# Performance work log

Measured on AMD Instinct MI355X. Metric: run time of the kernel, lower is better.

The kernel has to match this reference:

```python
import jax, jax.numpy as jnp
import numpy as np

EMBED_DIM = 768
NUM_HEADS = 12
HEAD_DIM = EMBED_DIM // NUM_HEADS


def setup_inputs() -> dict:
    key = jax.random.key(0)
    ks = jax.random.split(key, 9)
    B, S, E = 8, 1024, EMBED_DIM
    scale = 1.0 / np.sqrt(E)
    inputs = jax.random.normal(ks[0], (B, S, E), dtype=jnp.float32)
    Wq = jax.random.normal(ks[1], (E, E), dtype=jnp.float32) * scale
    Wk = jax.random.normal(ks[2], (E, E), dtype=jnp.float32) * scale
    Wv = jax.random.normal(ks[3], (E, E), dtype=jnp.float32) * scale
    Wo = jax.random.normal(ks[4], (E, E), dtype=jnp.float32) * scale
    bq = jnp.zeros((E,), dtype=jnp.float32)
    bk = jnp.zeros((E,), dtype=jnp.float32)
    bv = jnp.zeros((E,), dtype=jnp.float32)
    bo = jnp.zeros((E,), dtype=jnp.float32)
    return {"inputs": inputs, "Wq": Wq, "bq": bq, "Wk": Wk, "bk": bk,
            "Wv": Wv, "bv": bv, "Wo": Wo, "bo": bo}


def reference(inputs, Wq, bq, Wk, bk, Wv, bv, Wo, bo):
    B, S, E = inputs.shape
    H, D = NUM_HEADS, HEAD_DIM

    def split_heads(x):  # [B,S,E] -> [B,H,S,D]
        return x.reshape(B, S, H, D).transpose(0, 2, 1, 3)

    q = split_heads(inputs @ Wq + bq)
    k = split_heads(inputs @ Wk + bk)
    v = split_heads(inputs @ Wv + bv)

    # scaled dot-product attention; note: scale uses sqrt(last dim of key) = sqrt(D)
    score = jnp.einsum('bhqd,bhkd->bhqk', q, k) / jnp.sqrt(jnp.float32(D))
    weights = jax.nn.softmax(score, axis=-1)
    attn = jnp.einsum('bhqk,bhkd->bhqd', weights, v)  # [B,H,S,D]

    concat = attn.transpose(0, 2, 1, 3).reshape(B, S, E)
    return concat @ Wo + bo
```

## Files before the change

### kernel.cpp

```cpp
#include <hip/hip_runtime.h>
#include <hip/hip_bf16.h>
#include <cstddef>

#define E_DIM  768
#define S_LEN  1024
#define NHEADS 12
#define HDIM   64
#define BATCH  8
#define TOKENS (BATCH * S_LEN)
#define WELEMS (E_DIM * E_DIM)

typedef short bf16x8 __attribute__((ext_vector_type(8)));
typedef short bf16x4 __attribute__((ext_vector_type(4)));
typedef float f32x4  __attribute__((ext_vector_type(4)));

#define MFMA16(a, b, c)   __builtin_amdgcn_mfma_f32_16x16x32_bf16((a), (b), (c), 0, 0, 0)
#define MFMA16K16(a, b, c) __builtin_amdgcn_mfma_f32_16x16x16bf16_1k((a), (b), (c), 0, 0, 0)

#define GLD_LDS16(gp, lp)                                                  \
    __builtin_amdgcn_global_load_lds(                                      \
        (const __attribute__((address_space(1))) void*)(gp),               \
        (__attribute__((address_space(3))) void*)(lp), 16, 0, 0)

#define QSCALE 0.180336880f

static __device__ __forceinline__ short f2bf(float f) {
    union { float f; unsigned int u; } cv; cv.f = f;
    unsigned int u = cv.u + 0x7fffu + ((cv.u >> 16) & 1u);
    return (short)(u >> 16);
}

static __device__ __forceinline__ unsigned int pk2(float f0, float f1) {
    union { float f; unsigned int u; } a, b;
    a.f = f0; b.f = f1;
    return __builtin_amdgcn_perm(b.u + 0x8000u, a.u + 0x8000u, 0x07060302u);
}
static __device__ __forceinline__ bf16x4 pk4(float f0, float f1, float f2, float f3) {
    union { unsigned int u[2]; bf16x4 v; } r;
    r.u[0] = pk2(f0, f1); r.u[1] = pk2(f2, f3);
    return r.v;
}

__global__ __launch_bounds__(256) void xcvt_kernel(
    const float* __restrict__ X, short* __restrict__ Y)
{
    const size_t i = ((size_t)blockIdx.x * 256 + threadIdx.x) * 8;
    const float4 a = *(const float4*)&X[i];
    const float4 b = *(const float4*)&X[i + 4];
    union { unsigned int u[4]; bf16x8 v; } o;
    o.u[0] = pk2(a.x, a.y); o.u[1] = pk2(a.z, a.w);
    o.u[2] = pk2(b.x, b.y); o.u[3] = pk2(b.z, b.w);
    *(bf16x8*)&Y[i] = o.v;
}

__global__ __launch_bounds__(256) void transpose_w(
    const float* __restrict__ s0, const float* __restrict__ s1,
    const float* __restrict__ s2, const float* __restrict__ s3,
    short* __restrict__ dst)
{
    const int z = blockIdx.z;
    const float* S = (z == 0) ? s0 : (z == 1) ? s1 : (z == 2) ? s2 : s3;
    short* D = dst + (size_t)z * WELEMS;
    __shared__ float t[64][65];
    const int r = threadIdx.x >> 2, c0 = (threadIdx.x & 3) * 16;
    const int br = blockIdx.x * 64, bc = blockIdx.y * 64;
    #pragma unroll
    for (int j = 0; j < 4; ++j) {
        float4 v = *(const float4*)&S[(size_t)(br + r) * E_DIM + bc + c0 + j * 4];
        t[r][c0 + j * 4 + 0] = v.x; t[r][c0 + j * 4 + 1] = v.y;
        t[r][c0 + j * 4 + 2] = v.z; t[r][c0 + j * 4 + 3] = v.w;
    }
    __syncthreads();
    #pragma unroll
    for (int half = 0; half < 2; ++half) {
        union { unsigned int u[2]; bf16x4 v; } o0, o1;
        o0.u[0] = pk2(t[c0 + half * 8 + 0][r], t[c0 + half * 8 + 1][r]);
        o0.u[1] = pk2(t[c0 + half * 8 + 2][r], t[c0 + half * 8 + 3][r]);
        o1.u[0] = pk2(t[c0 + half * 8 + 4][r], t[c0 + half * 8 + 5][r]);
        o1.u[1] = pk2(t[c0 + half * 8 + 6][r], t[c0 + half * 8 + 7][r]);
        *(bf16x4*)&D[(size_t)(bc + r) * E_DIM + br + c0 + half * 8]     = o0.v;
        *(bf16x4*)&D[(size_t)(bc + r) * E_DIM + br + c0 + half * 8 + 4] = o1.v;
    }
}

template<bool AF32>
__global__ __launch_bounds__(256, 3) void gemm_qkv_t(
    const void* __restrict__ Ap, const short* __restrict__ Wt,
    const float* __restrict__ bq, const float* __restrict__ bk,
    const float* __restrict__ bv, short* __restrict__ oq,
    short* __restrict__ ok, short* __restrict__ ov)
{
    __shared__ __align__(16) short As[128 * 64];
    __shared__ __align__(16) short Bs[128 * 64];

    const int tid  = threadIdx.x;
    const int wave = tid >> 6, lane = tid & 63;
    const int quad = lane >> 4, l16 = lane & 15;
    const int bid = blockIdx.x;
    const int xcd = bid & 7, qq = bid >> 3;
    const int nblk = qq >> 3;
    const int bm = (xcd * 8 + (qq & 7)) * 128;
    const int wsel = nblk / 6;
    const int nb = (nblk % 6) * 128;
    const short* wt = Wt + (size_t)wsel * WELEMS;
    const float* bias = (wsel == 0) ? bq : (wsel == 1) ? bk : bv;
    short* outp = (wsel == 0) ? oq : (wsel == 1) ? ok : ov;
    const int wm = (wave >> 1) * 64, wn = (wave & 1) * 64;

    f32x4 acc[4][4];
    #pragma unroll
    for (int mt = 0; mt < 4; ++mt)
        #pragma unroll
        for (int nt = 0; nt < 4; ++nt) acc[mt][nt] = (f32x4){0.f, 0.f, 0.f, 0.f};

    for (int k0 = 0; k0 < E_DIM; k0 += 64) {
        if (AF32) {
            const float* A = (const float*)Ap;
            float4 ax[4][2];
            #pragma unroll
            for (int i = 0; i < 4; ++i) {
                const int slot = i * 256 + tid;
                const int row = slot >> 3, cl = slot & 7;
                const float4* gp = (const float4*)&A[(size_t)(bm + row) * E_DIM + k0 + cl * 8];
                ax[i][0] = gp[0]; ax[i][1] = gp[1];
            }
            __syncthreads();
            #pragma unroll
            for (int i = 0; i < 4; ++i) {
                const int slot = i * 256 + tid;
                const int row = slot >> 3, cl = slot & 7, cg = cl ^ (row & 7);
                GLD_LDS16(&wt[(size_t)(nb + row) * E_DIM + k0 + cg * 8], &Bs[slot * 8]);
            }
            #pragma unroll
            for (int i = 0; i < 4; ++i) {
                const int slot = i * 256 + tid;
                const int row = slot >> 3, cl = slot & 7, cs = cl ^ (row & 7);
                union { unsigned int u[4]; bf16x8 v; } v8;
                v8.u[0] = pk2(ax[i][0].x, ax[i][0].y);
                v8.u[1] = pk2(ax[i][0].z, ax[i][0].w);
                v8.u[2] = pk2(ax[i][1].x, ax[i][1].y);
                v8.u[3] = pk2(ax[i][1].z, ax[i][1].w);
                *(bf16x8*)&As[row * 64 + cs * 8] = v8.v;
            }
        } else {
            const short* A = (const short*)Ap;
            __syncthreads();
            #pragma unroll
            for (int i = 0; i < 4; ++i) {
                const int slot = i * 256 + tid;
                const int row = slot >> 3, cl = slot & 7, cg = cl ^ (row & 7);
                GLD_LDS16(&A[(size_t)(bm + row) * E_DIM + k0 + cg * 8], &As[slot * 8]);
            }
            #pragma unroll
            for (int i = 0; i < 4; ++i) {
                const int slot = i * 256 + tid;
                const int row = slot >> 3, cl = slot & 7, cg = cl ^ (row & 7);
                GLD_LDS16(&wt[(size_t)(nb + row) * E_DIM + k0 + cg * 8], &Bs[slot * 8]);
            }
        }
        __syncthreads();

        #pragma unroll
        for (int ks = 0; ks < 2; ++ks) {
            bf16x8 a[4], b[4];
            #pragma unroll
            for (int mt = 0; mt < 4; ++mt) {
                const int row = wm + mt * 16 + l16;
                const int c = (ks * 4 + quad) ^ (row & 7);
                a[mt] = *(const bf16x8*)&As[row * 64 + c * 8];
            }
            #pragma unroll
            for (int nt = 0; nt < 4; ++nt) {
                const int row = wn + nt * 16 + l16;
                const int c = (ks * 4 + quad) ^ (row & 7);
                b[nt] = *(const bf16x8*)&Bs[row * 64 + c * 8];
            }
            #pragma unroll
            for (int mt = 0; mt < 4; ++mt)
                #pragma unroll
                for (int nt = 0; nt < 4; ++nt)
                    acc[mt][nt] = MFMA16(a[mt], b[nt], acc[mt][nt]);
        }
    }

    const float qscale = (wsel == 0) ? QSCALE : 1.0f;
    #pragma unroll
    for (int nt = 0; nt < 4; ++nt) {
        const int ncol = nb + wn + nt * 16 + l16;
        const float bvv = bias[ncol];
        const int h = ncol >> 6, d = ncol & (HDIM - 1);
        #pragma unroll
        for (int mt = 0; mt < 4; ++mt) {
            const int grow = bm + wm + mt * 16 + quad * 4;
            if (wsel == 1) {
                #pragma unroll
                for (int r = 0; r < 4; ++r) {
                    const int g = grow + r, b = g >> 10, s = g & (S_LEN - 1);
                    outp[((size_t)(b * NHEADS + h) * S_LEN + s) * HDIM + d] =
                        f2bf(acc[mt][nt][r] + bvv);
                }
            } else {
                const int b = grow >> 10, s0 = grow & (S_LEN - 1);
                bf16x4 pv = pk4((acc[mt][nt][0] + bvv) * qscale,
                                (acc[mt][nt][1] + bvv) * qscale,
                                (acc[mt][nt][2] + bvv) * qscale,
                                (acc[mt][nt][3] + bvv) * qscale);
                *(bf16x4*)&outp[((size_t)(b * NHEADS + h) * HDIM + d) * S_LEN + s0] = pv;
            }
        }
    }
}

__global__ __launch_bounds__(256, 3) void gemm_out_kernel(
    const short* __restrict__ A, const short* __restrict__ Wt,
    const float* __restrict__ bias, float* __restrict__ out)
{
    __shared__ __align__(16) short As[128 * 64];
    __shared__ __align__(16) short Bs[128 * 64];

    const int tid  = threadIdx.x;
    const int wave = tid >> 6, lane = tid & 63;
    const int quad = lane >> 4, l16 = lane & 15;
    const int bid = blockIdx.x;
    const int xcd = bid & 7, qq = bid >> 3;
    const int nb = (qq >> 3) * 128;
    const int bm = (xcd * 8 + (qq & 7)) * 128;
    const int wm = (wave >> 1) * 64, wn = (wave & 1) * 64;

    f32x4 acc[4][4];
    #pragma unroll
    for (int mt = 0; mt < 4; ++mt)
        #pragma unroll
        for (int nt = 0; nt < 4; ++nt) acc[mt][nt] = (f32x4){0.f, 0.f, 0.f, 0.f};

    for (int k0 = 0; k0 < E_DIM; k0 += 64) {
        __syncthreads();
        #pragma unroll
        for (int i = 0; i < 4; ++i) {
            const int slot = i * 256 + tid;
            const int row = slot >> 3, cl = slot & 7, cg = cl ^ (row & 7);
            GLD_LDS16(&A[(size_t)(bm + row) * E_DIM + k0 + cg * 8], &As[slot * 8]);
        }
        #pragma unroll
        for (int i = 0; i < 4; ++i) {
            const int slot = i * 256 + tid;
            const int row = slot >> 3, cl = slot & 7, cg = cl ^ (row & 7);
            GLD_LDS16(&Wt[(size_t)(nb + row) * E_DIM + k0 + cg * 8], &Bs[slot * 8]);
        }
        __syncthreads();

        #pragma unroll
        for (int ks = 0; ks < 2; ++ks) {
            bf16x8 a[4], b[4];
            #pragma unroll
            for (int mt = 0; mt < 4; ++mt) {
                const int row = wm + mt * 16 + l16;
                const int c = (ks * 4 + quad) ^ (row & 7);
                a[mt] = *(const bf16x8*)&As[row * 64 + c * 8];
            }
            #pragma unroll
            for (int nt = 0; nt < 4; ++nt) {
                const int row = wn + nt * 16 + l16;
                const int c = (ks * 4 + quad) ^ (row & 7);
                b[nt] = *(const bf16x8*)&Bs[row * 64 + c * 8];
            }
            #pragma unroll
            for (int mt = 0; mt < 4; ++mt)
                #pragma unroll
                for (int nt = 0; nt < 4; ++nt)
                    acc[mt][nt] = MFMA16(a[mt], b[nt], acc[mt][nt]);
        }
    }

    #pragma unroll
    for (int nt = 0; nt < 4; ++nt) {
        const int ncol = nb + wn + nt * 16 + l16;
        const float bvv = bias[ncol];
        #pragma unroll
        for (int mt = 0; mt < 4; ++mt) {
            const int grow = bm + wm + mt * 16 + quad * 4;
            #pragma unroll
            for (int r = 0; r < 4; ++r)
                out[(size_t)(grow + r) * E_DIM + ncol] = acc[mt][nt][r] + bvv;
        }
    }
}

__global__ __launch_bounds__(256) void attn_kernel(
    const short* __restrict__ Q, const short* __restrict__ K,
    const short* __restrict__ V, short* __restrict__ O)
{
    __shared__ __align__(16) short Ks[2][64 * 64];
    __shared__ __align__(16) short Vt[2][64 * 64];

    const int tid  = threadIdx.x;
    const int wave = tid >> 6, lane = tid & 63;
    const int quad = lane >> 4, l16 = lane & 15;
    const int bh = blockIdx.x;
    const int q0 = blockIdx.y * 128;
    const size_t base = (size_t)bh * S_LEN * HDIM;
    const short* Qb = Q + base;
    const short* Kb = K + base;
    const short* Vb = V + base;

    bf16x8 qa[2][2];
    #pragma unroll
    for (int mt = 0; mt < 2; ++mt)
        #pragma unroll
        for (int ks = 0; ks < 2; ++ks) {
            const int s = q0 + wave * 32 + mt * 16 + l16;
            #pragma unroll
            for (int j = 0; j < 8; ++j)
                qa[mt][ks][j] = Qb[(size_t)(ks * 32 + quad * 8 + j) * S_LEN + s];
        }

    bf16x4 ones4;
    #pragma unroll
    for (int j = 0; j < 4; ++j) ones4[j] = (short)0x3F80;

    f32x4 oacc[2][4], lacc[2];
    #pragma unroll
    for (int mt = 0; mt < 2; ++mt) {
        #pragma unroll
        for (int nt = 0; nt < 4; ++nt) oacc[mt][nt] = (f32x4){0.f, 0.f, 0.f, 0.f};
        lacc[mt] = (f32x4){0.f, 0.f, 0.f, 0.f};
    }

    #pragma unroll
    for (int i = 0; i < 2; ++i) {
        const int slot = i * 256 + tid;
        const int row = slot >> 3, cl = slot & 7, cg = cl ^ (row & 7);
        GLD_LDS16(&Kb[(size_t)row * HDIM + cg * 8], &Ks[0][slot * 8]);
        GLD_LDS16(&Vb[(size_t)row * S_LEN + cg * 8], &Vt[0][slot * 8]);
    }

    for (int it = 0; it < S_LEN / 64; ++it) {
        __syncthreads();
        if (it + 1 < S_LEN / 64) {
            const int kt = (it + 1) * 64, nbf = (it + 1) & 1;
            #pragma unroll
            for (int i = 0; i < 2; ++i) {
                const int slot = i * 256 + tid;
                const int row = slot >> 3, cl = slot & 7, cg = cl ^ (row & 7);
                GLD_LDS16(&Kb[(size_t)(kt + row) * HDIM + cg * 8], &Ks[nbf][slot * 8]);
                GLD_LDS16(&Vb[(size_t)row * S_LEN + kt + cg * 8], &Vt[nbf][slot * 8]);
            }
        }
        const short* ksb = Ks[it & 1];
        const short* vtb = Vt[it & 1];

        f32x4 sc[2][4];
        #pragma unroll
        for (int mt = 0; mt < 2; ++mt)
            #pragma unroll
            for (int t = 0; t < 4; ++t) sc[mt][t] = (f32x4){0.f, 0.f, 0.f, 0.f};
        #pragma unroll
        for (int ks = 0; ks < 2; ++ks)
            #pragma unroll
            for (int t = 0; t < 4; ++t) {
                const int row = t * 16 + l16;
                const int c = (ks * 4 + quad) ^ (row & 7);
                const bf16x8 kf = *(const bf16x8*)&ksb[row * 64 + c * 8];
                #pragma unroll
                for (int mt = 0; mt < 2; ++mt)
                    sc[mt][t] = MFMA16(kf, qa[mt][ks], sc[mt][t]);
            }

        bf16x4 pa16[2][4];
        #pragma unroll
        for (int mt = 0; mt < 2; ++mt)
            #pragma unroll
            for (int t = 0; t < 4; ++t)
                pa16[mt][t] = pk4(__builtin_amdgcn_exp2f(sc[mt][t][0]),
                                  __builtin_amdgcn_exp2f(sc[mt][t][1]),
                                  __builtin_amdgcn_exp2f(sc[mt][t][2]),
                                  __builtin_amdgcn_exp2f(sc[mt][t][3]));

        #pragma unroll
        for (int t = 0; t < 4; ++t) {
            #pragma unroll
            for (int mt = 0; mt < 2; ++mt)
                lacc[mt] = MFMA16K16(pa16[mt][t], ones4, lacc[mt]);
            #pragma unroll
            for (int nt = 0; nt < 4; ++nt) {
                const int row = nt * 16 + l16;
                const int c = (t * 2 + (quad >> 1)) ^ (row & 7);
                const bf16x4 vb = *(const bf16x4*)&vtb[row * 64 + c * 8 + (quad & 1) * 4];
                #pragma unroll
                for (int mt = 0; mt < 2; ++mt)
                    oacc[mt][nt] = MFMA16K16(pa16[mt][t], vb, oacc[mt][nt]);
            }
        }
    }

    const int b = bh / NHEADS, h = bh - b * NHEADS;
    #pragma unroll
    for (int mt = 0; mt < 2; ++mt)
        #pragma unroll
        for (int nt = 0; nt < 4; ++nt)
            #pragma unroll
            for (int r = 0; r < 4; ++r) {
                const int qrow = q0 + wave * 32 + mt * 16 + quad * 4 + r;
                const float val = oacc[mt][nt][r] / lacc[mt][r];
                O[(size_t)(b * S_LEN + qrow) * E_DIM + h * HDIM + nt * 16 + l16] = f2bf(val);
            }
}

extern "C" void kernel_launch(void* const* d_in, const int* in_sizes, int n_in,
                              void* d_out, int out_size, void* d_ws, size_t ws_size,
                              hipStream_t stream) {
    const float* X  = (const float*)d_in[0];
    const float* Wq = (const float*)d_in[1];
    const float* bq = (const float*)d_in[2];
    const float* Wk = (const float*)d_in[3];
    const float* bk = (const float*)d_in[4];
    const float* Wv = (const float*)d_in[5];
    const float* bv = (const float*)d_in[6];
    const float* Wo = (const float*)d_in[7];
    const float* bo = (const float*)d_in[8];
    float* out = (float*)d_out;

    const size_t t = (size_t)TOKENS * E_DIM;
    short* q    = (short*)d_ws;
    short* k    = q + t;
    short* vT   = k + t;
    short* attn = vT + t;

    const size_t fast_need = (5 * t + 4 * (size_t)WELEMS) * 2;
    if (ws_size >= fast_need) {
        short* wt4 = attn + t;
        short* xbf = wt4 + 4 * (size_t)WELEMS;
        xcvt_kernel<<<(TOKENS * E_DIM / 8) / 256, 256, 0, stream>>>(X, xbf);
        transpose_w<<<dim3(12, 12, 4), 256, 0, stream>>>(Wq, Wk, Wv, Wo, wt4);
        gemm_qkv_t<false><<<1152, 256, 0, stream>>>(
            xbf, wt4, bq, bk, bv, q, k, vT);
        attn_kernel<<<dim3(BATCH * NHEADS, S_LEN / 128), 256, 0, stream>>>(q, k, vT, attn);
        gemm_out_kernel<<<384, 256, 0, stream>>>(
            attn, wt4 + 3 * (size_t)WELEMS, bo, out);
    } else {
        short* wt_qkv = attn;
        short* wt_o   = q;
        transpose_w<<<dim3(12, 12, 3), 256, 0, stream>>>(Wq, Wk, Wv, Wv, wt_qkv);
        gemm_qkv_t<true><<<1152, 256, 0, stream>>>(
            X, wt_qkv, bq, bk, bv, q, k, vT);
        attn_kernel<<<dim3(BATCH * NHEADS, S_LEN / 128), 256, 0, stream>>>(q, k, vT, attn);
        transpose_w<<<dim3(12, 12, 1), 256, 0, stream>>>(Wo, Wo, Wo, Wo, wt_o);
        gemm_out_kernel<<<384, 256, 0, stream>>>(attn, wt_o, bo, out);
    }
}
```

Measured before the change: 191.6 us.

## Double-buffer LDS tiles in QKV and output projection GEMMs

Adds a second LDS buffer for the A and B tiles in both projection GEMMs. The next k-tile is issued before computing on the current one, so global loads overlap MFMA work and one barrier per iteration is dropped. This doubles shared memory per block, which can reduce how many blocks fit on a CU. In the fp32-input path the synchronous register loads still stall before compute.

```diff
diff --git a/kernel.cpp b/kernel.cpp
--- a/kernel.cpp
+++ b/kernel.cpp
@@ -90,8 +90,8 @@
     const float* __restrict__ bv, short* __restrict__ oq,
     short* __restrict__ ok, short* __restrict__ ov)
 {
-    __shared__ __align__(16) short As[128 * 64];
-    __shared__ __align__(16) short Bs[128 * 64];
+    __shared__ __align__(16) short As[2][128 * 64];
+    __shared__ __align__(16) short Bs[2][128 * 64];
 
     const int tid  = threadIdx.x;
     const int wave = tid >> 6, lane = tid & 63;
@@ -113,52 +113,53 @@
         #pragma unroll
         for (int nt = 0; nt < 4; ++nt) acc[mt][nt] = (f32x4){0.f, 0.f, 0.f, 0.f};
 
-    for (int k0 = 0; k0 < E_DIM; k0 += 64) {
+    const int NIT = E_DIM / 64;
+
+    auto stage = [&](int it, int bf) {
+        const int k0 = it * 64;
         if (AF32) {
             const float* A = (const float*)Ap;
-            float4 ax[4][2];
-            #pragma unroll
-            for (int i = 0; i < 4; ++i) {
-                const int slot = i * 256 + tid;
-                const int row = slot >> 3, cl = slot & 7;
-                const float4* gp = (const float4*)&A[(size_t)(bm + row) * E_DIM + k0 + cl * 8];
-                ax[i][0] = gp[0]; ax[i][1] = gp[1];
-            }
-            __syncthreads();
             #pragma unroll
             for (int i = 0; i < 4; ++i) {
                 const int slot = i * 256 + tid;
                 const int row = slot >> 3, cl = slot & 7, cg = cl ^ (row & 7);
-                GLD_LDS16(&wt[(size_t)(nb + row) * E_DIM + k0 + cg * 8], &Bs[slot * 8]);
+                GLD_LDS16(&wt[(size_t)(nb + row) * E_DIM + k0 + cg * 8], &Bs[bf][slot * 8]);
             }
             #pragma unroll
             for (int i = 0; i < 4; ++i) {
                 const int slot = i * 256 + tid;
                 const int row = slot >> 3, cl = slot & 7, cs = cl ^ (row & 7);
+                const float4* gp = (const float4*)&A[(size_t)(bm + row) * E_DIM + k0 + cl * 8];
+                const float4 a0 = gp[0], a1 = gp[1];
                 union { unsigned int u[4]; bf16x8 v; } v8;
-                v8.u[0] = pk2(ax[i][0].x, ax[i][0].y);
-                v8.u[1] = pk2(ax[i][0].z, ax[i][0].w);
-                v8.u[2] = pk2(ax[i][1].x, ax[i][1].y);
-                v8.u[3] = pk2(ax[i][1].z, ax[i][1].w);
-                *(bf16x8*)&As[row * 64 + cs * 8] = v8.v;
+                v8.u[0] = pk2(a0.x, a0.y); v8.u[1] = pk2(a0.z, a0.w);
+                v8.u[2] = pk2(a1.x, a1.y); v8.u[3] = pk2(a1.z, a1.w);
+                *(bf16x8*)&As[bf][row * 64 + cs * 8] = v8.v;
             }
         } else {
             const short* A = (const short*)Ap;
-            __syncthreads();
             #pragma unroll
             for (int i = 0; i < 4; ++i) {
                 const int slot = i * 256 + tid;
                 const int row = slot >> 3, cl = slot & 7, cg = cl ^ (row & 7);
-                GLD_LDS16(&A[(size_t)(bm + row) * E_DIM + k0 + cg * 8], &As[slot * 8]);
+                GLD_LDS16(&A[(size_t)(bm + row) * E_DIM + k0 + cg * 8], &As[bf][slot * 8]);
             }
             #pragma unroll
             for (int i = 0; i < 4; ++i) {
                 const int slot = i * 256 + tid;
                 const int row = slot >> 3, cl = slot & 7, cg = cl ^ (row & 7);
-                GLD_LDS16(&wt[(size_t)(nb + row) * E_DIM + k0 + cg * 8], &Bs[slot * 8]);
-            }
-        }
+                GLD_LDS16(&wt[(size_t)(nb + row) * E_DIM + k0 + cg * 8], &Bs[bf][slot * 8]);
+            }
+        }
+    };
+
+    stage(0, 0);
+
+    for (int it = 0; it < NIT; ++it) {
         __syncthreads();
+        if (it + 1 < NIT) stage(it + 1, (it + 1) & 1);
+        const short* as = As[it & 1];
+        const short* bs = Bs[it & 1];
 
         #pragma unroll
         for (int ks = 0; ks < 2; ++ks) {
@@ -167,13 +168,13 @@
             for (int mt = 0; mt < 4; ++mt) {
                 const int row = wm + mt * 16 + l16;
                 const int c = (ks * 4 + quad) ^ (row & 7);
-                a[mt] = *(const bf16x8*)&As[row * 64 + c * 8];
+                a[mt] = *(const bf16x8*)&as[row * 64 + c * 8];
             }
             #pragma unroll
             for (int nt = 0; nt < 4; ++nt) {
                 const int row = wn + nt * 16 + l16;
                 const int c = (ks * 4 + quad) ^ (row & 7);
-                b[nt] = *(const bf16x8*)&Bs[row * 64 + c * 8];
+                b[nt] = *(const bf16x8*)&bs[row * 64 + c * 8];
             }
             #pragma unroll
             for (int mt = 0; mt < 4; ++mt)
@@ -215,8 +216,8 @@
     const short* __restrict__ A, const short* __restrict__ Wt,
     const float* __restrict__ bias, float* __restrict__ out)
 {
-    __shared__ __align__(16) short As[128 * 64];
-    __shared__ __align__(16) short Bs[128 * 64];
+    __shared__ __align__(16) short As[2][128 * 64];
+    __shared__ __align__(16) short Bs[2][128 * 64];
 
     const int tid  = threadIdx.x;
     const int wave = tid >> 6, lane = tid & 63;
@@ -233,21 +234,31 @@
         #pragma unroll
         for (int nt = 0; nt < 4; ++nt) acc[mt][nt] = (f32x4){0.f, 0.f, 0.f, 0.f};
 
-    for (int k0 = 0; k0 < E_DIM; k0 += 64) {
-        __syncthreads();
+    const int NIT = E_DIM / 64;
+
+    auto stage = [&](int it, int bf) {
+        const int k0 = it * 64;
         #pragma unroll
         for (int i = 0; i < 4; ++i) {
             const int slot = i * 256 + tid;
             const int row = slot >> 3, cl = slot & 7, cg = cl ^ (row & 7);
-            GLD_LDS16(&A[(size_t)(bm + row) * E_DIM + k0 + cg * 8], &As[slot * 8]);
+            GLD_LDS16(&A[(size_t)(bm + row) * E_DIM + k0 + cg * 8], &As[bf][slot * 8]);
         }
         #pragma unroll
         for (int i = 0; i < 4; ++i) {
             const int slot = i * 256 + tid;
             const int row = slot >> 3, cl = slot & 7, cg = cl ^ (row & 7);
-            GLD_LDS16(&Wt[(size_t)(nb + row) * E_DIM + k0 + cg * 8], &Bs[slot * 8]);
-        }
+            GLD_LDS16(&Wt[(size_t)(nb + row) * E_DIM + k0 + cg * 8], &Bs[bf][slot * 8]);
+        }
+    };
+
+    stage(0, 0);
+
+    for (int it = 0; it < NIT; ++it) {
         __syncthreads();
+        if (it + 1 < NIT) stage(it + 1, (it + 1) & 1);
+        const short* as = As[it & 1];
+        const short* bs = Bs[it & 1];
 
         #pragma unroll
         for (int ks = 0; ks < 2; ++ks) {
@@ -256,13 +267,13 @@
             for (int mt = 0; mt < 4; ++mt) {
                 const int row = wm + mt * 16 + l16;
                 const int c = (ks * 4 + quad) ^ (row & 7);
-                a[mt] = *(const bf16x8*)&As[row * 64 + c * 8];
+                a[mt] = *(const bf16x8*)&as[row * 64 + c * 8];
             }
             #pragma unroll
             for (int nt = 0; nt < 4; ++nt) {
                 const int row = wn + nt * 16 + l16;
                 const int c = (ks * 4 + quad) ^ (row & 7);
-                b[nt] = *(const bf16x8*)&Bs[row * 64 + c * 8];
+                b[nt] = *(const bf16x8*)&bs[row * 64 + c * 8];
             }
             #pragma unroll
             for (int mt = 0; mt < 4; ++mt)
```

Result: slower. 206.2 us (+7.6%).
